# Kernel optimization log

Measured on AMD Instinct MI355X. Metric: run time of the kernel, lower is better.

## Reference

```python
import jax, jax.numpy as jnp
import numpy as np

EPS = 1e-12  # F.normalize default eps


def setup_inputs() -> dict:
    key = jax.random.key(0)
    k1, k2 = jax.random.split(key)
    E, N, B, T, Fdim, K = 2, 512, 64, 12, 2, 64
    supports = jax.random.uniform(k1, (E, N, N), dtype=jnp.float32)
    inputs = jax.random.normal(k2, (B, T, N, Fdim), dtype=jnp.float32)
    bias = jnp.ones((E, K), dtype=jnp.float32)  # init.ones_
    # torch.svd at __init__: A = u @ diag(s) @ v^T, truncated to node_dim
    u_np, s_np, vh_np = np.linalg.svd(np.asarray(supports), full_matrices=False)
    u = jnp.asarray(u_np[..., :K])                      # [E, N, K]
    s = jnp.asarray(s_np[..., :K])                      # [E, K]
    v = jnp.asarray(np.swapaxes(vh_np, -1, -2)[..., :K])  # [E, N, K]
    return {"supports": supports, "u": u, "s": s, "v": v, "bias": bias, "inputs": inputs}


def _pairwise_dist(x):
    # x: [B, N, T] L2-normalized rows; returns [B, N, N] Euclidean distances
    sq = jnp.sum(x * x, axis=-1)                      # [B, N]
    inner = jnp.einsum('bnt,bmt->bnm', x, x)          # [B, N, N]
    d2 = jnp.maximum(sq[:, :, None] + sq[:, None, :] - 2.0 * inner, 0.0)
    # safe sqrt (zero on the diagonal, matching torch.cdist)
    pos = d2 > 0
    return jnp.where(pos, jnp.sqrt(jnp.where(pos, d2, 1.0)), 0.0)


def reference(supports, u, s, v, bias, inputs):
    # SAdaptor: low-rank SVD reconstruction with softplus-scaled singular values
    s_scaled = s * jax.nn.softplus(bias)              # [E, K]
    adaptive = jnp.einsum('enk,ek,emk->enm', u, s_scaled, v)  # [E, N, N]
    sup = supports + adaptive                         # [E, N, N]

    # TAdaptor: exp(-cdist) of L2-normalized node histories (dropout: eval mode)
    x = jnp.transpose(inputs[..., 0], (0, 2, 1))      # [B, N, T]
    nrm = jnp.sqrt(jnp.sum(x * x, axis=-1, keepdims=True))
    nodes = x / jnp.maximum(nrm, EPS)                 # F.normalize(p=2)
    dynamic = jnp.exp(-_pairwise_dist(nodes))         # [B, N, N]

    out = sup[:, None, :, :] * (dynamic[None] + 1.0)  # [E, B, N, N]
    out = jax.nn.relu(out)
    # F.normalize(p=1, dim=-1); out >= 0 so |out| == out
    return out / jnp.maximum(jnp.sum(out, axis=-1, keepdims=True), EPS)
```

## Files before the change

kernel.cpp:

```cpp
#include <hip/hip_runtime.h>
#include <hip/hip_bf16.h>

#define E 2
#define N 512
#define B 64
#define T 12
#define K 64
#define NB 4

__global__ __launch_bounds__(512)
void k_sup(const float* __restrict__ supports, const float* __restrict__ uu,
           const float* __restrict__ ss, const float* __restrict__ vv,
           const float* __restrict__ bias, float* __restrict__ sup) {
    const int en = blockIdx.x;
    const int e = en >> 9, n = en & (N - 1);
    __shared__ float uls[K];
    const int tid = threadIdx.x;
    if (tid < K) {
        float uf = uu[(size_t)(e * N + n) * K + tid];
        float sf = ss[e * K + tid];
        float bb = bias[e * K + tid];
        float sp = (bb > 0.f) ? (bb + log1pf(expf(-bb))) : log1pf(expf(bb));
        uls[tid] = uf * sf * sp;
    }
    __syncthreads();
    const int m = tid;
    const float4* vp = reinterpret_cast<const float4*>(vv + (size_t)(e * N + m) * K);
    float acc = 0.f;
#pragma unroll
    for (int i = 0; i < 16; ++i) {
        float4 q = vp[i];
        const float* w = &uls[i * 4];
        acc += w[0] * q.x + w[1] * q.y + w[2] * q.z + w[3] * q.w;
    }
    const size_t o = (size_t)(e * N + n) * N + m;
    sup[o] = acc + supports[o];
}

__global__ __launch_bounds__(256)
void k_nodes(const float* __restrict__ inp, float* __restrict__ nodes) {
    const int idx = blockIdx.x * 256 + threadIdx.x;
    const int b = idx >> 9, n = idx & (N - 1);
    float x[T];
    float sq = 0.f;
#pragma unroll
    for (int t = 0; t < T; ++t) {
        float xv = inp[((size_t)(b * T + t) * N + n) * 2];
        x[t] = xv;
        sq += xv * xv;
    }
    float inv = 1.f / fmaxf(sqrtf(sq), 1e-12f);
#pragma unroll
    for (int t = 0; t < T; ++t) nodes[(size_t)idx * T + t] = x[t] * inv;
}

__global__ __launch_bounds__(512)
void k_main(const float* __restrict__ sup, const float* __restrict__ nodes,
            float* __restrict__ out) {
    const int bi = blockIdx.x;
    const int b = bi >> 7;
    const int n0 = (bi & 127) * NB;
    const int m = threadIdx.x;

    __shared__ float an[NB][T];
    __shared__ float red0[8], red1[8];
    __shared__ float invs[2];

    float r[T];
    const float4* np4 = reinterpret_cast<const float4*>(nodes + (size_t)(b * N + m) * T);
    float4 q0 = np4[0], q1 = np4[1], q2 = np4[2];
    r[0] = q0.x; r[1] = q0.y; r[2]  = q0.z; r[3]  = q0.w;
    r[4] = q1.x; r[5] = q1.y; r[6]  = q1.z; r[7]  = q1.w;
    r[8] = q2.x; r[9] = q2.y; r[10] = q2.z; r[11] = q2.w;

    if ((unsigned)(m - n0) < NB) {
#pragma unroll
        for (int t = 0; t < T; ++t) an[m - n0][t] = r[t];
    }
    __syncthreads();

#pragma unroll
    for (int j = 0; j < NB; ++j) {
        const int n = n0 + j;
        float d2 = 0.f;
#pragma unroll
        for (int t = 0; t < T; ++t) {
            float d = r[t] - an[j][t];
            d2 += d * d;
        }
        float dist = (d2 > 0.f) ? sqrtf(d2) : 0.f;
        float dynp1 = __expf(-dist) + 1.f;

        float v0 = fmaxf(sup[(size_t)(0 * N + n) * N + m] * dynp1, 0.f);
        float v1 = fmaxf(sup[(size_t)(1 * N + n) * N + m] * dynp1, 0.f);

        float s0 = v0, s1 = v1;
#pragma unroll
        for (int off = 32; off > 0; off >>= 1) {
            s0 += __shfl_down(s0, off);
            s1 += __shfl_down(s1, off);
        }
        const int wave = m >> 6, lane = m & 63;
        if (lane == 0) { red0[wave] = s0; red1[wave] = s1; }
        __syncthreads();
        if (m == 0) {
            float t0 = 0.f, t1 = 0.f;
#pragma unroll
            for (int w = 0; w < 8; ++w) { t0 += red0[w]; t1 += red1[w]; }
            invs[0] = 1.f / fmaxf(t0, 1e-12f);
            invs[1] = 1.f / fmaxf(t1, 1e-12f);
        }
        __syncthreads();

        const size_t o0 = ((size_t)(0 * B + b) * N + n) * N + m;
        const size_t o1 = ((size_t)(1 * B + b) * N + n) * N + m;
        out[o0] = v0 * invs[0];
        out[o1] = v1 * invs[1];
    }
}

extern "C" void kernel_launch(void* const* d_in, const int* in_sizes, int n_in,
                              void* d_out, int out_size, void* d_ws, size_t ws_size,
                              hipStream_t stream) {
    const float* supports = (const float*)d_in[0];
    const float* uu       = (const float*)d_in[1];
    const float* ss       = (const float*)d_in[2];
    const float* vv       = (const float*)d_in[3];
    const float* bias     = (const float*)d_in[4];
    const float* inp      = (const float*)d_in[5];
    float* out = (float*)d_out;

    float* sup   = (float*)d_ws;
    float* nodes = sup + (size_t)E * N * N;

    k_sup  <<<E * N,        512, 0, stream>>>(supports, uu, ss, vv, bias, sup);
    k_nodes<<<(B * N) / 256, 256, 0, stream>>>(inp, nodes);
    k_main <<<B * (N / NB), 512, 0, stream>>>(sup, nodes, out);
}
```

Before: 197.5 us.

## Fuse prep kernels and batch row reductions with DPP wave sums

Merges the low-rank support reconstruction and node normalization into one prep launch, with each support block now computing four rows so every v load is reused across those rows. The main kernel loads all support values up front and computes all eight row sums with DPP-based wave reductions. It then finishes them with a single pair of barriers instead of two barriers per row. This cuts launch count, barrier stalls and serialized global loads, at the cost of more registers per thread.

```diff
diff --git a/kernel.cpp b/kernel.cpp
--- a/kernel.cpp
+++ b/kernel.cpp
@@ -1,5 +1,4 @@
 #include <hip/hip_runtime.h>
-#include <hip/hip_bf16.h>
 
 #define E 2
 #define N 512
@@ -8,50 +7,71 @@
 #define K 64
 #define NB 4
 
-__global__ __launch_bounds__(512)
-void k_sup(const float* __restrict__ supports, const float* __restrict__ uu,
-           const float* __restrict__ ss, const float* __restrict__ vv,
-           const float* __restrict__ bias, float* __restrict__ sup) {
-    const int en = blockIdx.x;
-    const int e = en >> 9, n = en & (N - 1);
-    __shared__ float uls[K];
-    const int tid = threadIdx.x;
-    if (tid < K) {
-        float uf = uu[(size_t)(e * N + n) * K + tid];
-        float sf = ss[e * K + tid];
-        float bb = bias[e * K + tid];
-        float sp = (bb > 0.f) ? (bb + log1pf(expf(-bb))) : log1pf(expf(bb));
-        uls[tid] = uf * sf * sp;
-    }
-    __syncthreads();
-    const int m = tid;
-    const float4* vp = reinterpret_cast<const float4*>(vv + (size_t)(e * N + m) * K);
-    float acc = 0.f;
-#pragma unroll
-    for (int i = 0; i < 16; ++i) {
-        float4 q = vp[i];
-        const float* w = &uls[i * 4];
-        acc += w[0] * q.x + w[1] * q.y + w[2] * q.z + w[3] * q.w;
-    }
-    const size_t o = (size_t)(e * N + n) * N + m;
-    sup[o] = acc + supports[o];
+template<int CTRL, int RM>
+__device__ __forceinline__ float dpp_add(float x) {
+    int y = __builtin_amdgcn_update_dpp(0, __float_as_int(x), CTRL, RM, 0xf, true);
+    return x + __int_as_float(y);
+}
+__device__ __forceinline__ float wave_sum64(float x) {
+    x = dpp_add<0x111, 0xf>(x);
+    x = dpp_add<0x112, 0xf>(x);
+    x = dpp_add<0x114, 0xf>(x);
+    x = dpp_add<0x118, 0xf>(x);
+    x = dpp_add<0x142, 0xa>(x);
+    x = dpp_add<0x143, 0xc>(x);
+    return __int_as_float(__builtin_amdgcn_readlane(__float_as_int(x), 63));
 }
 
-__global__ __launch_bounds__(256)
-void k_nodes(const float* __restrict__ inp, float* __restrict__ nodes) {
-    const int idx = blockIdx.x * 256 + threadIdx.x;
-    const int b = idx >> 9, n = idx & (N - 1);
-    float x[T];
-    float sq = 0.f;
+__global__ __launch_bounds__(512)
+void k_prep(const float* __restrict__ supports, const float* __restrict__ uu,
+            const float* __restrict__ ss, const float* __restrict__ vv,
+            const float* __restrict__ bias, const float* __restrict__ inp,
+            float* __restrict__ sup, float* __restrict__ nodes) {
+    const int blk = blockIdx.x;
+    const int tid = threadIdx.x;
+    if (blk < 2 * (N / NB)) {
+        const int e = blk >> 7;
+        const int n0 = (blk & 127) * NB;
+        __shared__ float uls[NB][K];
+        if (tid < NB * K) {
+            const int j = tid >> 6, k = tid & 63;
+            float bb = bias[e * K + k];
+            float sp_ = (bb > 0.f) ? (bb + log1pf(expf(-bb))) : log1pf(expf(bb));
+            uls[j][k] = uu[(size_t)(e * N + n0 + j) * K + k] * ss[e * K + k] * sp_;
+        }
+        __syncthreads();
+        const int m = tid;
+        const float4* vp = reinterpret_cast<const float4*>(vv + (size_t)(e * N + m) * K);
+        float accs[NB] = {0.f, 0.f, 0.f, 0.f};
 #pragma unroll
-    for (int t = 0; t < T; ++t) {
-        float xv = inp[((size_t)(b * T + t) * N + n) * 2];
-        x[t] = xv;
-        sq += xv * xv;
+        for (int i = 0; i < 16; ++i) {
+            float4 q = vp[i];
+#pragma unroll
+            for (int j = 0; j < NB; ++j) {
+                const float* w = &uls[j][i * 4];
+                accs[j] += w[0] * q.x + w[1] * q.y + w[2] * q.z + w[3] * q.w;
+            }
+        }
+#pragma unroll
+        for (int j = 0; j < NB; ++j) {
+            const size_t o = (size_t)(e * N + n0 + j) * N + m;
+            sup[o] = accs[j] + supports[o];
+        }
+    } else {
+        const int idx = (blk - 2 * (N / NB)) * 512 + tid;
+        const int b = idx >> 9, n = idx & (N - 1);
+        float x[T];
+        float sq = 0.f;
+#pragma unroll
+        for (int t = 0; t < T; ++t) {
+            float xv = inp[((size_t)(b * T + t) * N + n) * 2];
+            x[t] = xv;
+            sq += xv * xv;
+        }
+        float inv = 1.f / fmaxf(sqrtf(sq), 1e-12f);
+#pragma unroll
+        for (int t = 0; t < T; ++t) nodes[(size_t)idx * T + t] = x[t] * inv;
     }
-    float inv = 1.f / fmaxf(sqrtf(sq), 1e-12f);
-#pragma unroll
-    for (int t = 0; t < T; ++t) nodes[(size_t)idx * T + t] = x[t] * inv;
 }
 
 __global__ __launch_bounds__(512)
@@ -61,61 +81,63 @@
     const int b = bi >> 7;
     const int n0 = (bi & 127) * NB;
     const int m = threadIdx.x;
+    const int wave = m >> 6, lane = m & 63;
 
-    __shared__ float an[NB][T];
-    __shared__ float red0[8], red1[8];
-    __shared__ float invs[2];
+    __shared__ float red[8 * 8];
+    __shared__ float invs[8];
 
-    float r[T];
     const float4* np4 = reinterpret_cast<const float4*>(nodes + (size_t)(b * N + m) * T);
     float4 q0 = np4[0], q1 = np4[1], q2 = np4[2];
-    r[0] = q0.x; r[1] = q0.y; r[2]  = q0.z; r[3]  = q0.w;
-    r[4] = q1.x; r[5] = q1.y; r[6]  = q1.z; r[7]  = q1.w;
-    r[8] = q2.x; r[9] = q2.y; r[10] = q2.z; r[11] = q2.w;
+    float r[T] = {q0.x, q0.y, q0.z, q0.w, q1.x, q1.y, q1.z, q1.w, q2.x, q2.y, q2.z, q2.w};
 
-    if ((unsigned)(m - n0) < NB) {
+    const float* __restrict__ anc = nodes + (size_t)(b * N + n0) * T;
+
+    float sp[NB][2];
 #pragma unroll
-        for (int t = 0; t < T; ++t) an[m - n0][t] = r[t];
+    for (int j = 0; j < NB; ++j) {
+        sp[j][0] = sup[(size_t)(n0 + j) * N + m];
+        sp[j][1] = sup[(size_t)(N + n0 + j) * N + m];
+    }
+
+    float v[NB][2];
+#pragma unroll
+    for (int j = 0; j < NB; ++j) {
+        float d2 = 0.f;
+#pragma unroll
+        for (int t = 0; t < T; ++t) {
+            float d = r[t] - anc[j * T + t];
+            d2 += d * d;
+        }
+        float dist = (d2 > 0.f) ? sqrtf(d2) : 0.f;
+        float f = __expf(-dist) + 1.f;
+        v[j][0] = fmaxf(sp[j][0] * f, 0.f);
+        v[j][1] = fmaxf(sp[j][1] * f, 0.f);
+    }
+
+#pragma unroll
+    for (int j = 0; j < NB; ++j) {
+#pragma unroll
+        for (int e = 0; e < 2; ++e) {
+            float tot = wave_sum64(v[j][e]);
+            if (lane == 0) red[wave * 8 + j * 2 + e] = tot;
+        }
+    }
+    __syncthreads();
+    if (wave == 0) {
+        float t = red[lane];
+        t += __shfl_xor(t, 8);
+        t += __shfl_xor(t, 16);
+        t += __shfl_xor(t, 32);
+        if (lane < 8) invs[lane] = 1.f / fmaxf(t, 1e-12f);
     }
     __syncthreads();
 
 #pragma unroll
     for (int j = 0; j < NB; ++j) {
-        const int n = n0 + j;
-        float d2 = 0.f;
 #pragma unroll
-        for (int t = 0; t < T; ++t) {
-            float d = r[t] - an[j][t];
-            d2 += d * d;
+        for (int e = 0; e < 2; ++e) {
+            out[((size_t)(e * B + b) * N + n0 + j) * N + m] = v[j][e] * invs[j * 2 + e];
         }
-        float dist = (d2 > 0.f) ? sqrtf(d2) : 0.f;
-        float dynp1 = __expf(-dist) + 1.f;
-
-        float v0 = fmaxf(sup[(size_t)(0 * N + n) * N + m] * dynp1, 0.f);
-        float v1 = fmaxf(sup[(size_t)(1 * N + n) * N + m] * dynp1, 0.f);
-
-        float s0 = v0, s1 = v1;
-#pragma unroll
-        for (int off = 32; off > 0; off >>= 1) {
-            s0 += __shfl_down(s0, off);
-            s1 += __shfl_down(s1, off);
-        }
-        const int wave = m >> 6, lane = m & 63;
-        if (lane == 0) { red0[wave] = s0; red1[wave] = s1; }
-        __syncthreads();
-        if (m == 0) {
-            float t0 = 0.f, t1 = 0.f;
-#pragma unroll
-            for (int w = 0; w < 8; ++w) { t0 += red0[w]; t1 += red1[w]; }
-            invs[0] = 1.f / fmaxf(t0, 1e-12f);
-            invs[1] = 1.f / fmaxf(t1, 1e-12f);
-        }
-        __syncthreads();
-
-        const size_t o0 = ((size_t)(0 * B + b) * N + n) * N + m;
-        const size_t o1 = ((size_t)(1 * B + b) * N + n) * N + m;
-        out[o0] = v0 * invs[0];
-        out[o1] = v1 * invs[1];
     }
 }
 
@@ -133,7 +155,7 @@
     float* sup   = (float*)d_ws;
     float* nodes = sup + (size_t)E * N * N;
 
-    k_sup  <<<E * N,        512, 0, stream>>>(supports, uu, ss, vv, bias, sup);
-    k_nodes<<<(B * N) / 256, 256, 0, stream>>>(inp, nodes);
-    k_main <<<B * (N / NB), 512, 0, stream>>>(sup, nodes, out);
+    k_prep<<<2 * (N / NB) + (B * N) / 512, 512, 0, stream>>>(
+        supports, uu, ss, vv, bias, inp, sup, nodes);
+    k_main<<<B * (N / NB), 512, 0, stream>>>(sup, nodes, out);
 }
```

Result: faster. 170.0 us (-14.0%).
